# Kernel tuning notes

Measured on AMD Instinct MI355X. Metric: run time of the kernel, lower is better.

The kernel has to match this reference:

```python
import jax, jax.numpy as jnp
import numpy as np

N_TOKENS = 100000
CUT = [0, 20000, 50000, 100000]  # cutoff_ends
D = 1024


def setup_inputs() -> dict:
    key = jax.random.key(0)
    ks = jax.random.split(key, 12)
    B, S = 2, 1024
    hidden = jax.random.normal(ks[0], (B, S, D), dtype=jnp.float32)
    target = jax.random.randint(ks[1], (B, S), 0, N_TOKENS, dtype=jnp.int64)
    s = 0.02
    # cluster 0 (shortlist) + cluster projection head
    w0 = jax.random.normal(ks[2], (20000, 1024), dtype=jnp.float32) * s
    b0 = jnp.zeros((20000,), jnp.float32)
    cluster_w = jax.random.normal(ks[3], (2, 1024), dtype=jnp.float32) * s  # n_clusters=2
    cluster_b = jnp.zeros((2,), jnp.float32)
    proj0 = jax.random.normal(ks[4], (1024, 1024), dtype=jnp.float32) * s  # d_proj x d_emb_0
    # tail cluster 1: d_emb_1 = 1024 // 4 = 256, vocab slice 20000..50000
    w1 = jax.random.normal(ks[5], (30000, 256), dtype=jnp.float32) * s
    b1 = jnp.zeros((30000,), jnp.float32)
    proj1 = jax.random.normal(ks[6], (1024, 256), dtype=jnp.float32) * s
    # tail cluster 2: d_emb_2 = 1024 // 16 = 64, vocab slice 50000..100000
    w2 = jax.random.normal(ks[7], (50000, 64), dtype=jnp.float32) * s
    b2 = jnp.zeros((50000,), jnp.float32)
    proj2 = jax.random.normal(ks[8], (1024, 64), dtype=jnp.float32) * s
    return {"hidden": hidden, "target": target,
            "w0": w0, "b0": b0, "cluster_w": cluster_w, "cluster_b": cluster_b, "proj0": proj0,
            "w1": w1, "b1": b1, "proj1": proj1,
            "w2": w2, "b2": b2, "proj2": proj2}


def reference(hidden, target, w0, b0, cluster_w, cluster_b, proj0,
              w1, b1, proj1, w2, b2, proj2):
    tgt_shape = target.shape
    h = hidden.reshape(-1, D)            # [N, d_proj]
    t = target.reshape(-1)               # [N]

    # head: shortlist logits + cluster logits, via low-rank projection
    head_w = jnp.concatenate([w0, cluster_w], axis=0)   # [20002, 1024]
    head_b = jnp.concatenate([b0, cluster_b], axis=0)
    head_logit = (h @ proj0) @ head_w.T + head_b        # [N, 20002]
    head_lp = jax.nn.log_softmax(head_logit, axis=1)

    nll = jnp.zeros(t.shape, h.dtype)

    # cluster 0 (shortlist): logprob is head_lp at the target id
    m0 = t < CUT[1]
    idx0 = jnp.clip(t, 0, CUT[1] - 1)
    lp0 = jnp.take_along_axis(head_lp, idx0[:, None], axis=1)[:, 0]
    nll = jnp.where(m0, -lp0, nll)

    # tail clusters. NOTE: faithful to original quirk head_logprob[:, -i]
    tails = [(CUT[1], CUT[2], w1, b1, proj1), (CUT[2], CUT[3], w2, b2, proj2)]
    for i, (left, right, w, b, p) in enumerate(tails, start=1):
        m = (t >= left) & (t < right)
        tail_logit = (h @ p) @ w.T + b                  # [N, right-left]
        tail_lp = jax.nn.log_softmax(tail_logit, axis=1)
        ti = jnp.clip(t - left, 0, right - left - 1)
        lp = head_lp[:, -i] + jnp.take_along_axis(tail_lp, ti[:, None], axis=1)[:, 0]
        nll = jnp.where(m, -lp, nll)

    return nll.reshape(tgt_shape)
```

## Files before the change

### kernel.cpp

```cpp
#include <hip/hip_runtime.h>
#include <cstdint>
#include <cstddef>

#define DEV static __device__ __forceinline__

typedef __attribute__((ext_vector_type(8))) short bf16x8_t;
typedef __attribute__((ext_vector_type(4))) float f32x4_t;

DEV unsigned short f2bf(float f) {
  union { float f; unsigned u; } v; v.f = f;
  unsigned r = v.u + 0x7fffu + ((v.u >> 16) & 1u);
  return (unsigned short)(r >> 16);
}

DEV void gl_lds16(const void* g, void* l) {
  __builtin_amdgcn_global_load_lds(
      (const __attribute__((address_space(1))) void*)g,
      (__attribute__((address_space(3))) void*)l,
      16, 0, 0);
}

__global__ __launch_bounds__(256)
void prep_k(const int* __restrict__ target,
            int* __restrict__ idx1, int* __restrict__ pos1,
            int* __restrict__ idx2, int* __restrict__ pos2,
            int* __restrict__ cnts,
            const float* __restrict__ p0, const float* __restrict__ p1,
            const float* __restrict__ p2, unsigned short* __restrict__ pAll,
            const float* __restrict__ s0, unsigned short* __restrict__ d0, int n0,
            const float* __restrict__ s1, unsigned short* __restrict__ d1, int n1,
            const float* __restrict__ s2, unsigned short* __restrict__ d2, int n2,
            const float* __restrict__ s3, unsigned short* __restrict__ d3, int n3,
            const float* __restrict__ s4, unsigned short* __restrict__ d4, int n4) {
  const int bid = blockIdx.x;
  const int tid = threadIdx.x;
  if (bid == 0) {
    __shared__ int c1, c2;
    if (tid == 0) { c1 = 0; c2 = 0; }
    __syncthreads();
    for (int i = tid; i < 2048; i += 256) {
      int t = target[i];
      if (t >= 20000 && t < 50000) {
        int p = atomicAdd(&c1, 1); idx1[p] = i; pos1[i] = p;
      } else if (t >= 50000) {
        int p = atomicAdd(&c2, 1); idx2[p] = i; pos2[i] = p;
      }
    }
    __syncthreads();
    if (tid == 0) { cnts[0] = c1; cnts[1] = c2; }
    return;
  }
  if (bid <= 1344) {
    __shared__ float tile[32][33];
    int b = bid - 1;
    const float* src; unsigned short* dst; int C, bx, by;
    if (b < 1024)      { src = p0; dst = pAll;               C = 1024; bx = b % 32; by = b / 32; }
    else if (b < 1280) { int q = b - 1024; src = p1; dst = pAll + 1024 * 1024; C = 256; bx = q % 8; by = q / 8; }
    else               { int q = b - 1280; src = p2; dst = pAll + 1280 * 1024; C = 64;  bx = q % 2; by = q / 2; }
    const int R = 1024;
    int tx = tid & 31, ty = tid >> 5;
    int c0 = bx * 32, r0 = by * 32;
    for (int yy = ty; yy < 32; yy += 8)
      tile[yy][tx] = src[(size_t)(r0 + yy) * C + (c0 + tx)];
    __syncthreads();
    for (int yy = ty; yy < 32; yy += 8)
      dst[(size_t)(c0 + yy) * R + (r0 + tx)] = f2bf(tile[tx][yy]);
    return;
  }
  int j = (bid - 1345) * 256 + tid;
  const float* s; unsigned short* d;
  if (j < n0) { s = s0; d = d0; }
  else { j -= n0;
    if (j < n1) { s = s1; d = d1; }
    else { j -= n1;
      if (j < n2) { s = s2; d = d2; }
      else { j -= n2;
        if (j < n3) { s = s3; d = d3; }
        else { j -= n3; if (j >= n4) return; s = s4; d = d4; }
      }
    }
  }
  float4 f = ((const float4*)s)[j];
  ushort4 o;
  o.x = f2bf(f.x); o.y = f2bf(f.y); o.z = f2bf(f.z); o.w = f2bf(f.w);
  ((ushort4*)d)[j] = o;
}

__global__ __launch_bounds__(256)
void proj_gemm_k(const unsigned short* __restrict__ A,
                 const unsigned short* __restrict__ W,
                 unsigned short* __restrict__ Cout) {
  __shared__ __align__(16) unsigned short As[128 * 32];
  __shared__ __align__(16) unsigned short Bs[128 * 32];
  const int K = 1024, V = 1344;
  const int tm = blockIdx.x, tn = blockIdx.y;
  const int m0 = tm * 128, n0 = tn * 128;
  const int tid = threadIdx.x, wid = tid >> 6, lane = tid & 63;
  const int quad = lane >> 4, l16 = lane & 15;
  const int wr = wid >> 1, wc = wid & 1;

  f32x4_t acc[4][4];
  const f32x4_t zero4 = {0.f, 0.f, 0.f, 0.f};
#pragma unroll
  for (int i = 0; i < 4; ++i)
#pragma unroll
    for (int j = 0; j < 4; ++j) acc[i][j] = zero4;

  const int srow = wid * 32 + (lane >> 2);
  const int skk  = (lane & 3) * 8;
  const unsigned short* Ap0 = A + (size_t)(m0 + srow) * K + skk;
  const unsigned short* Ap1 = A + (size_t)(m0 + srow + 16) * K + skk;
  int wrow0 = n0 + srow;      if (wrow0 > V - 1) wrow0 = V - 1;
  int wrow1 = n0 + srow + 16; if (wrow1 > V - 1) wrow1 = V - 1;
  const unsigned short* Wp0 = W + (size_t)wrow0 * K + skk;
  const unsigned short* Wp1 = W + (size_t)wrow1 * K + skk;
  unsigned short* Asw = As + wid * 1024;
  unsigned short* Bsw = Bs + wid * 1024;

  for (int k0 = 0; k0 < K; k0 += 32) {
    gl_lds16(Ap0, Asw);
    gl_lds16(Ap1, Asw + 512);
    gl_lds16(Wp0, Bsw);
    gl_lds16(Wp1, Bsw + 512);
    Ap0 += 32; Ap1 += 32; Wp0 += 32; Wp1 += 32;
    __syncthreads();
    bf16x8_t af[4], bfr[4];
#pragma unroll
    for (int i = 0; i < 4; ++i)
      af[i] = *(const bf16x8_t*)(As + (size_t)(wr * 64 + i * 16 + l16) * 32 + quad * 8);
#pragma unroll
    for (int j = 0; j < 4; ++j)
      bfr[j] = *(const bf16x8_t*)(Bs + (size_t)(wc * 64 + j * 16 + l16) * 32 + quad * 8);
#pragma unroll
    for (int i = 0; i < 4; ++i)
#pragma unroll
      for (int j = 0; j < 4; ++j)
        acc[i][j] = __builtin_amdgcn_mfma_f32_16x16x32_bf16(af[i], bfr[j], acc[i][j], 0, 0, 0);
    __syncthreads();
  }
#pragma unroll
  for (int i = 0; i < 4; ++i)
#pragma unroll
    for (int j = 0; j < 4; ++j) {
      const int n = n0 + wc * 64 + j * 16 + l16;
      if (n < V) {
#pragma unroll
        for (int r = 0; r < 4; ++r) {
          const int m = m0 + wr * 64 + i * 16 + quad * 4 + r;
          Cout[(size_t)m * V + n] = f2bf(acc[i][j][r]);
        }
      }
    }
}


#define SBAR() __builtin_amdgcn_s_barrier()

#define STA(BUF, HALF, KT)                                                    \
  {                                                                           \
    const unsigned short* g_ = aB0 + (size_t)(HALF) * (128 * 1344) + (KT) * 64; \
    char* d_ = (char*)SA[BUF][HALF] + ldsw;                                   \
    gl_lds16(g_, d_);                                                         \
    gl_lds16(g_ + 64 * 1344, d_ + 8192);                                      \
  }

#define STB(BUF, HALF, KT)                                                    \
  {                                                                           \
    char* d_ = (char*)SB[BUF][HALF] + ldsw;                                   \
    gl_lds16(bP##HALF##0 + (KT) * 64, d_);                                    \
    gl_lds16(bP##HALF##1 + (KT) * 64, d_ + 8192);                             \
  }

#define MMQ(mb, nb, BB)                                                       \
  {                                                                           \
    _Pragma("unroll") for (int mi = 0; mi < 4; ++mi) {                        \
      _Pragma("unroll") for (int nj = 0; nj < 2; ++nj) {                      \
        acc[(mb) + mi][(nb) + nj] = __builtin_amdgcn_mfma_f32_16x16x32_bf16(  \
            Af[0][mi], BB[0][nj], acc[(mb) + mi][(nb) + nj], 0, 0, 0);        \
        acc[(mb) + mi][(nb) + nj] = __builtin_amdgcn_mfma_f32_16x16x32_bf16(  \
            Af[1][mi], BB[1][nj], acc[(mb) + mi][(nb) + nj], 0, 0, 0);        \
      }                                                                       \
    }                                                                         \
  }

#define PH(D_, E_, KTV)                                                       \
  {                                                                           \
    const int kt_ = (KTV);                                                    \
    const int t1_ = (kt_ + 1 > 15) ? 15 : (kt_ + 1);                          \
    const int t2_ = (kt_ + 2 > 15) ? 15 : (kt_ + 2);                          \
              \
    _Pragma("unroll") for (int mi = 0; mi < 4; ++mi) {                        \
      Af[0][mi] = *(const bf16x8_t*)(pa##D_##a + mi * 2048);                  \
      Af[1][mi] = *(const bf16x8_t*)(pa##D_##b + mi * 2048);                  \
    }                                                                         \
    _Pragma("unroll") for (int nj = 0; nj < 2; ++nj) {                        \
      Bh[0][nj] = *(const bf16x8_t*)(pb##D_##a + (2 + nj) * 2048);            \
      Bh[1][nj] = *(const bf16x8_t*)(pb##D_##b + (2 + nj) * 2048);            \
    }                                                                         \
    STB(E_, 1, t1_);                                                          \
    __builtin_amdgcn_s_setprio(1); MMQ(0, 0, Bl); __builtin_amdgcn_s_setprio(0); \
    SBAR();                                                                   \
              \
    __builtin_amdgcn_s_setprio(1); MMQ(0, 2, Bh); __builtin_amdgcn_s_setprio(0); \
    _Pragma("unroll") for (int mi = 0; mi < 4; ++mi) {                        \
      Af[0][mi] = *(const bf16x8_t*)(pa##D_##a + (4 + mi) * 2048);            \
      Af[1][mi] = *(const bf16x8_t*)(pa##D_##b + (4 + mi) * 2048);            \
    }                                                                         \
    STA(E_, 1, t1_);                                                          \
    SBAR();                                                                   \
               \
    STB(D_, 0, t2_);                                                          \
    __builtin_amdgcn_s_setprio(1); MMQ(4, 0, Bl); __builtin_amdgcn_s_setprio(0); \
    asm volatile("s_waitcnt vmcnt(2)" ::: "memory");                          \
    SBAR();                                                                   \
           \
    STA(D_, 0, t2_);                                                          \
    _Pragma("unroll") for (int nj = 0; nj < 2; ++nj) {                        \
      Bl[0][nj] = *(const bf16x8_t*)(pb##E_##a + nj * 2048);                  \
      Bl[1][nj] = *(const bf16x8_t*)(pb##E_##b + nj * 2048);                  \
    }                                                                         \
    __builtin_amdgcn_s_setprio(1); MMQ(4, 2, Bh); __builtin_amdgcn_s_setprio(0); \
    SBAR();                                                                   \
  }

#define PROLOGUE6()                                                           \
  { STB(0, 0, 0); STA(0, 0, 0); STB(0, 1, 0); STA(0, 1, 0);                   \
    STB(1, 0, 1); STA(1, 0, 1); }

typedef unsigned short lds_half_t[2][8192];

DEV void head_body(char* UB, int bid,
                   const unsigned short* __restrict__ Pall,
                   const unsigned short* __restrict__ w0b,
                   const float* __restrict__ b0, const float* __restrict__ cb,
                   float* __restrict__ part0, float* __restrict__ g0,
                   float* __restrict__ cg, const int* __restrict__ target) {
  lds_half_t* SA = (lds_half_t*)UB;
  lds_half_t* SB = (lds_half_t*)(UB + 65536);

  const int V = 20002;
  const int orig = (bid & 7) * 79 + (bid >> 3);
  const int mt = orig & 7, stripe = orig >> 3;
  const int m0 = mt * 256, n0 = stripe * 256;

  const int tid = threadIdx.x;
  const int wid = tid >> 6, lane = tid & 63;
  const int quad = lane >> 4, l16 = lane & 15;
  const int wr = wid >> 2, wc = wid & 3;

  const int r0  = tid >> 3;
  const int ibh = ((tid & 7) ^ (r0 & 7)) << 3;

  const unsigned short* aB0 = Pall + (size_t)(m0 + r0) * 1344 + ibh;
  int br00 = n0 + r0;            if (br00 > V - 1) br00 = V - 1;
  int br01 = n0 + r0 + 64;       if (br01 > V - 1) br01 = V - 1;
  int br10 = n0 + 128 + r0;      if (br10 > V - 1) br10 = V - 1;
  int br11 = n0 + 128 + r0 + 64; if (br11 > V - 1) br11 = V - 1;
  const unsigned short* bP00 = w0b + (size_t)br00 * 1024 + ibh;
  const unsigned short* bP01 = w0b + (size_t)br01 * 1024 + ibh;
  const unsigned short* bP10 = w0b + (size_t)br10 * 1024 + ibh;
  const unsigned short* bP11 = w0b + (size_t)br11 * 1024 + ibh;

  const int ldsw = wid * 1024;

  const int aoff0 = l16 * 128 + ((quad ^ (l16 & 3)) << 4) + (((l16 >> 2) & 1) << 6);
  const int aoff1 = aoff0 ^ 64;
  const char* pa0a = (const char*)SA[0][wr] + aoff0;
  const char* pa0b = (const char*)SA[0][wr] + aoff1;
  const char* pa1a = (const char*)SA[1][wr] + aoff0;
  const char* pa1b = (const char*)SA[1][wr] + aoff1;
  const char* pb0a = (const char*)SB[0][wc >> 1] + (wc & 1) * 8192 + aoff0;
  const char* pb0b = (const char*)SB[0][wc >> 1] + (wc & 1) * 8192 + aoff1;
  const char* pb1a = (const char*)SB[1][wc >> 1] + (wc & 1) * 8192 + aoff0;
  const char* pb1b = (const char*)SB[1][wc >> 1] + (wc & 1) * 8192 + aoff1;

  f32x4_t acc[8][4];
  const f32x4_t zero4 = {0.f, 0.f, 0.f, 0.f};
#pragma unroll
  for (int i = 0; i < 8; ++i)
#pragma unroll
    for (int j = 0; j < 4; ++j) acc[i][j] = zero4;

  bf16x8_t Af[2][4];
  bf16x8_t Bl[2][2];
  bf16x8_t Bh[2][2];

  PROLOGUE6();
  asm volatile("s_waitcnt vmcnt(4)" ::: "memory");
  SBAR();
#pragma unroll
  for (int nj = 0; nj < 2; ++nj) {
    Bl[0][nj] = *(const bf16x8_t*)(pb0a + nj * 2048);
    Bl[1][nj] = *(const bf16x8_t*)(pb0b + nj * 2048);
  }

#pragma unroll 1
  for (int ktp = 0; ktp < 8; ++ktp) {
    const int kt0 = 2 * ktp;
    PH(0, 1, kt0);
    PH(1, 0, kt0 + 1);
  }

  asm volatile("s_waitcnt vmcnt(0) lgkmcnt(0)" ::: "memory");
  SBAR();

  int nj[4]; float bj[4];
#pragma unroll
  for (int j = 0; j < 4; ++j) {
    nj[j] = n0 + wc * 64 + j * 16 + l16;
    bj[j] = (nj[j] < 20000) ? b0[nj[j]] : ((nj[j] < V) ? cb[nj[j] - 20000] : 0.f);
  }
  float* redf = (float*)UB;
#pragma unroll
  for (int i = 0; i < 8; ++i) {
#pragma unroll
    for (int r = 0; r < 4; ++r) {
      const int rloc = i * 16 + quad * 4 + r;
      const int token = m0 + wr * 128 + rloc;
      float v[4], sum = 0.f;
#pragma unroll
      for (int j = 0; j < 4; ++j) {
        v[j] = acc[i][j][r] + bj[j];
        if (nj[j] < V) sum += __expf(v[j]);
      }
#pragma unroll
      for (int off = 1; off < 16; off <<= 1)
        sum += __shfl_xor(sum, off, 64);
      if (l16 == 0) redf[(wr * 4 + wc) * 128 + rloc] = sum;
      const int t = target[token];
      const int gi = (t < 19999) ? t : 19999;
#pragma unroll
      for (int j = 0; j < 4; ++j) {
        if (nj[j] == gi) g0[token] = v[j];
        if (nj[j] == 20000) cg[2 * token]     = v[j];
        if (nj[j] == 20001) cg[2 * token + 1] = v[j];
      }
    }
  }
  __syncthreads();
  if (tid < 256) {
    const int wrr = tid >> 7, rr = tid & 127;
    const float s = redf[(wrr * 4 + 0) * 128 + rr] + redf[(wrr * 4 + 1) * 128 + rr]
                  + redf[(wrr * 4 + 2) * 128 + rr] + redf[(wrr * 4 + 3) * 128 + rr];
    part0[(size_t)(m0 + tid) * 79 + stripe] = s;
  }
}

#undef PH
#undef MMQ
#undef STA
#undef STB
#undef PROLOGUE6
#undef SBAR

template <int KT>
DEV void tail_body8(char* UB, int tn,
                    const unsigned short* __restrict__ A, int ldA,
                    const unsigned short* __restrict__ W,
                    const float* __restrict__ bias, int V, int nt2x,
                    const int* __restrict__ rowidx,
                    const int* __restrict__ cnt_ptr,
                    float* __restrict__ partials,
                    float* __restrict__ gathered,
                    const int* __restrict__ target, int glo) {
  constexpr int KC  = KT / 64;
  constexpr int NCB = KT / 32;
  unsigned short* Bs = (unsigned short*)UB;
  char* AsB = UB + NCB * 8192;

  const int n0 = tn * 128;
  const int Meff = *cnt_ptr;
  const int tid = threadIdx.x;
  const int lane = tid & 63, wid = tid >> 6;
  const int quad = lane >> 4, l16 = lane & 15;
  const int wr = wid >> 1, wc = wid & 1;
  const int srow = tid >> 2;
  const int scol = (tid & 3) * 8;
  const int ldsw = wid * 1024;

  int wrow = n0 + srow; if (wrow > V - 1) wrow = V - 1;
#pragma unroll
  for (int c = 0; c < NCB; ++c)
    gl_lds16(W + (size_t)wrow * KT + c * 32 + scol, (char*)Bs + c * 8192 + ldsw);

  int nj[4]; float bj[4];
#pragma unroll
  for (int j = 0; j < 4; ++j) {
    nj[j] = n0 + wc * 64 + j * 16 + l16;
    bj[j] = (nj[j] < V) ? bias[nj[j]] : 0.f;
  }

  const int nm = (Meff + 255) >> 8;
  const int S = nm * KC;

  auto stageA = [&](int s, int buf) {
    const int m = s / KC, k = s - m * KC;
#pragma unroll
    for (int cc = 0; cc < 2; ++cc)
#pragma unroll
      for (int h = 0; h < 2; ++h) {
        int ar = m * 256 + srow + h * 128;
        if (ar > Meff - 1) ar = Meff - 1;
        if (ar < 0) ar = 0;
        const int Arow = rowidx[ar];
        gl_lds16(A + (size_t)Arow * ldA + k * 64 + cc * 32 + scol,
                 AsB + buf * 32768 + cc * 16384 + h * 8192 + ldsw);
      }
  };

  stageA(0, 0);
  __syncthreads();

  f32x4_t acc[4][4];
  const f32x4_t zero4 = {0.f, 0.f, 0.f, 0.f};

  for (int s = 0; s < S; ++s) {
    const int buf = s & 1;
    const int m = s / KC, k = s - m * KC;
    if (s + 1 < S) stageA(s + 1, buf ^ 1);
    if (k == 0) {
#pragma unroll
      for (int i = 0; i < 4; ++i)
#pragma unroll
        for (int j = 0; j < 4; ++j) acc[i][j] = zero4;
    }
#pragma unroll
    for (int cc = 0; cc < 2; ++cc) {
      bf16x8_t af[4], bfr[4];
#pragma unroll
      for (int i = 0; i < 4; ++i)
        af[i] = *(const bf16x8_t*)(AsB + buf * 32768 + cc * 16384 +
                                   (wr * 64 + i * 16 + l16) * 64 + quad * 16);
#pragma unroll
      for (int j = 0; j < 4; ++j)
        bfr[j] = *(const bf16x8_t*)((char*)Bs + (k * 2 + cc) * 8192 +
                                    (wc * 64 + j * 16 + l16) * 64 + quad * 16);
#pragma unroll
      for (int i = 0; i < 4; ++i)
#pragma unroll
        for (int j = 0; j < 4; ++j)
          acc[i][j] = __builtin_amdgcn_mfma_f32_16x16x32_bf16(af[i], bfr[j], acc[i][j], 0, 0, 0);
    }
    if (k == KC - 1) {
#pragma unroll
      for (int i = 0; i < 4; ++i) {
#pragma unroll
        for (int r = 0; r < 4; ++r) {
          const int row = wr * 64 + i * 16 + quad * 4 + r;
          const int gr = m * 256 + row;
          const int grc = (gr < Meff) ? gr : (Meff - 1);
          const int token = rowidx[grc];
          float v[4], sum = 0.f;
#pragma unroll
          for (int j = 0; j < 4; ++j) {
            v[j] = acc[i][j][r] + bj[j];
            if (nj[j] < V) sum += __expf(v[j]);
          }
#pragma unroll
          for (int off = 1; off < 16; off <<= 1)
            sum += __shfl_xor(sum, off, 64);
          if (l16 == 0)
            partials[(size_t)grc * nt2x + 2 * tn + wc] = sum;
          const int gi = target[token] - glo;
#pragma unroll
          for (int j = 0; j < 4; ++j)
            if (nj[j] == gi) gathered[token] = v[j];
        }
      }
    }
    __syncthreads();
  }
}

__global__ __launch_bounds__(512, 2)
void fused_k(const unsigned short* __restrict__ Pall,
             const unsigned short* __restrict__ w0b,
             const float* __restrict__ b0, const float* __restrict__ cb,
             float* __restrict__ part0, float* __restrict__ g0,
             float* __restrict__ cg, const int* __restrict__ target,
             const unsigned short* __restrict__ w1b, const float* __restrict__ b1,
             const int* __restrict__ idx1, const int* __restrict__ cnt1,
             float* __restrict__ part1, float* __restrict__ g1,
             const unsigned short* __restrict__ w2b, const float* __restrict__ b2,
             const int* __restrict__ idx2, const int* __restrict__ cnt2,
             float* __restrict__ part2, float* __restrict__ g2,
             int nt1x2, int nt2x2) {
  __shared__ __align__(16) char UB[132096];
  const int bid = blockIdx.x;
  if (bid < 632) {
    head_body(UB, bid, Pall, w0b, b0, cb, part0, g0, cg, target);
  } else if (bid < 632 + 235) {
    tail_body8<256>(UB, bid - 632, Pall + 1024, 1344, w1b, b1, 30000, nt1x2,
                    idx1, cnt1, part1, g1, target, 20000);
  } else {
    tail_body8<64>(UB, bid - 867, Pall + 1280, 1344, w2b, b2, 50000, nt2x2,
                   idx2, cnt2, part2, g2, target, 50000);
  }
}

__global__ __launch_bounds__(256)
void combine_k(const float* __restrict__ part0,
               const float* __restrict__ part1, int nt1,
               const float* __restrict__ part2, int nt2,
               const float* __restrict__ g0, const float* __restrict__ g1,
               const float* __restrict__ g2, const float* __restrict__ cg,
               const int* __restrict__ pos1, const int* __restrict__ pos2,
               const int* __restrict__ target, float* __restrict__ out) {
  const int w = threadIdx.x >> 6, lane = threadIdx.x & 63;
  const int token = blockIdx.x * 4 + w;
  const int t = target[token];

  float S = 0.f;
  for (int i = lane; i < 79; i += 64)
    S += part0[(size_t)token * 79 + i];
#pragma unroll
  for (int off = 1; off < 64; off <<= 1)
    S += __shfl_xor(S, off, 64);
  const float lse_head = __logf(S);

  float res;
  if (t < 20000) {
    res = lse_head - g0[token];
  } else {
    const float* pt; int nt; float gv, ch; int row;
    if (t < 50000) { pt = part1; nt = nt1; gv = g1[token]; ch = cg[2 * token + 1]; row = pos1[token]; }
    else           { pt = part2; nt = nt2; gv = g2[token]; ch = cg[2 * token];     row = pos2[token]; }
    float S2 = 0.f;
    for (int i = lane; i < nt; i += 64)
      S2 += pt[(size_t)row * nt + i];
#pragma unroll
    for (int off = 1; off < 64; off <<= 1)
      S2 += __shfl_xor(S2, off, 64);
    float lse_t = __logf(S2);
    res = -((ch - lse_head) + (gv - lse_t));
  }
  if (lane == 0) out[token] = res;
}

extern "C" void kernel_launch(void* const* d_in, const int* in_sizes, int n_in,
                              void* d_out, int out_size, void* d_ws, size_t ws_size,
                              hipStream_t stream) {
  (void)in_sizes; (void)n_in; (void)out_size; (void)ws_size;
  const float* hidden = (const float*)d_in[0];
  const int*   target = (const int*)d_in[1];
  const float* w0     = (const float*)d_in[2];
  const float* b0     = (const float*)d_in[3];
  const float* cw     = (const float*)d_in[4];
  const float* cb     = (const float*)d_in[5];
  const float* proj0  = (const float*)d_in[6];
  const float* w1     = (const float*)d_in[7];
  const float* b1     = (const float*)d_in[8];
  const float* proj1  = (const float*)d_in[9];
  const float* w2     = (const float*)d_in[10];
  const float* b2     = (const float*)d_in[11];
  const float* proj2  = (const float*)d_in[12];
  float* out = (float*)d_out;

  const int NT1 = 235, NT2 = 391;
  const int NT1X = 2 * NT1, NT2X = 2 * NT2;

  char* p = (char*)d_ws;
  auto alloc = [&](size_t bytes) {
    char* r = p; p += (bytes + 255) & ~(size_t)255; return r;
  };
  unsigned short* Hb   = (unsigned short*)alloc(2048ull * 1024 * 2);
  unsigned short* pAll = (unsigned short*)alloc(1344ull * 1024 * 2);
  unsigned short* w0b  = (unsigned short*)alloc(20002ull * 1024 * 2);
  unsigned short* w1b  = (unsigned short*)alloc(30000ull * 256 * 2);
  unsigned short* w2b  = (unsigned short*)alloc(50000ull * 64 * 2);
  unsigned short* Pall = (unsigned short*)alloc(2048ull * 1344 * 2);
  float* part0 = (float*)alloc(2048ull * 79 * 4);
  float* part1 = (float*)alloc(2048ull * NT1X * 4);
  float* part2 = (float*)alloc(2048ull * NT2X * 4);
  float* g0 = (float*)alloc(2048 * 4);
  float* g1 = (float*)alloc(2048 * 4);
  float* g2 = (float*)alloc(2048 * 4);
  float* cg = (float*)alloc(2048 * 2 * 4);
  int* idx1 = (int*)alloc(2048 * 4);
  int* pos1 = (int*)alloc(2048 * 4);
  int* idx2 = (int*)alloc(2048 * 4);
  int* pos2 = (int*)alloc(2048 * 4);
  int* cnts = (int*)alloc(2 * 4);

  const int c_h = 2048 * 1024 / 4, c_w0 = 20000 * 1024 / 4, c_cw = 2048 / 4,
            c_w1 = 30000 * 256 / 4, c_w2 = 50000 * 64 / 4;
  const int ctot = c_h + c_w0 + c_cw + c_w1 + c_w2;
  const int nb_cast = (ctot + 255) / 256;
  prep_k<<<1 + 1344 + nb_cast, 256, 0, stream>>>(
      target, idx1, pos1, idx2, pos2, cnts,
      proj0, proj1, proj2, pAll,
      hidden, Hb, c_h,
      w0, w0b, c_w0,
      cw, w0b + 20000ull * 1024, c_cw,
      w1, w1b, c_w1,
      w2, w2b, c_w2);

  proj_gemm_k<<<dim3(16, 11), 256, 0, stream>>>(Hb, pAll, Pall);

  fused_k<<<632 + NT1 + NT2, 512, 0, stream>>>(
      Pall, w0b, b0, cb, part0, g0, cg, target,
      w1b, b1, idx1, cnts + 0, part1, g1,
      w2b, b2, idx2, cnts + 1, part2, g2,
      NT1X, NT2X);

  combine_k<<<512, 256, 0, stream>>>(part0, part1, NT1X, part2, NT2X,
      g0, g1, g2, cg, pos1, pos2, target, out);
}
```

Before: 384.2 us.

## Overlap weight casts with projection GEMM and fold combine into fused kernel

Moves the bf16 casting of the vocabulary weights out of the prep kernel and into the projection GEMM launch as extra blocks, so the casts run alongside the GEMM instead of before it. Replaces the separate combine kernel with a tail in fused_k: each block takes a ticket from an atomic counter, and the last 32 blocks spin until all blocks finish, then do the per-token log-sum-exp combine. This removes one launch and one inter-kernel gap. It relies on the last-ticket blocks being resident while they wait, and on NB=1258 matching the actual grid size, which depends on NT1/NT2.

```diff
diff --git a/kernel.cpp b/kernel.cpp
--- a/kernel.cpp
+++ b/kernel.cpp
@@ -27,11 +27,7 @@
             int* __restrict__ cnts,
             const float* __restrict__ p0, const float* __restrict__ p1,
             const float* __restrict__ p2, unsigned short* __restrict__ pAll,
-            const float* __restrict__ s0, unsigned short* __restrict__ d0, int n0,
-            const float* __restrict__ s1, unsigned short* __restrict__ d1, int n1,
-            const float* __restrict__ s2, unsigned short* __restrict__ d2, int n2,
-            const float* __restrict__ s3, unsigned short* __restrict__ d3, int n3,
-            const float* __restrict__ s4, unsigned short* __restrict__ d4, int n4) {
+            const float* __restrict__ s0, unsigned short* __restrict__ d0, int n0) {
   const int bid = blockIdx.x;
   const int tid = threadIdx.x;
   if (bid == 0) {
@@ -47,7 +43,7 @@
       }
     }
     __syncthreads();
-    if (tid == 0) { cnts[0] = c1; cnts[1] = c2; }
+    if (tid == 0) { cnts[0] = c1; cnts[1] = c2; cnts[2] = 0; }
     return;
   }
   if (bid <= 1344) {
@@ -68,34 +64,47 @@
     return;
   }
   int j = (bid - 1345) * 256 + tid;
-  const float* s; unsigned short* d;
-  if (j < n0) { s = s0; d = d0; }
-  else { j -= n0;
-    if (j < n1) { s = s1; d = d1; }
-    else { j -= n1;
-      if (j < n2) { s = s2; d = d2; }
-      else { j -= n2;
-        if (j < n3) { s = s3; d = d3; }
-        else { j -= n3; if (j >= n4) return; s = s4; d = d4; }
-      }
-    }
-  }
-  float4 f = ((const float4*)s)[j];
+  if (j >= n0) return;
+  float4 f = ((const float4*)s0)[j];
   ushort4 o;
   o.x = f2bf(f.x); o.y = f2bf(f.y); o.z = f2bf(f.z); o.w = f2bf(f.w);
-  ((ushort4*)d)[j] = o;
+  ((ushort4*)d0)[j] = o;
 }
 
 __global__ __launch_bounds__(256)
-void proj_gemm_k(const unsigned short* __restrict__ A,
-                 const unsigned short* __restrict__ W,
-                 unsigned short* __restrict__ Cout) {
+void projcast_k(const unsigned short* __restrict__ A,
+                const unsigned short* __restrict__ W,
+                unsigned short* __restrict__ Cout,
+                const float* __restrict__ s0, unsigned short* __restrict__ d0, int n0,
+                const float* __restrict__ s1, unsigned short* __restrict__ d1, int n1,
+                const float* __restrict__ s2, unsigned short* __restrict__ d2, int n2,
+                const float* __restrict__ s3, unsigned short* __restrict__ d3, int n3) {
+  const int bid = blockIdx.x;
+  const int tid = threadIdx.x;
+  if (bid >= 176) {
+    int j = (bid - 176) * 256 + tid;
+    const float* s; unsigned short* d;
+    if (j < n0) { s = s0; d = d0; }
+    else { j -= n0;
+      if (j < n1) { s = s1; d = d1; }
+      else { j -= n1;
+        if (j < n2) { s = s2; d = d2; }
+        else { j -= n2; if (j >= n3) return; s = s3; d = d3; }
+      }
+    }
+    float4 f = ((const float4*)s)[j];
+    ushort4 o;
+    o.x = f2bf(f.x); o.y = f2bf(f.y); o.z = f2bf(f.z); o.w = f2bf(f.w);
+    ((ushort4*)d)[j] = o;
+    return;
+  }
+
   __shared__ __align__(16) unsigned short As[128 * 32];
   __shared__ __align__(16) unsigned short Bs[128 * 32];
   const int K = 1024, V = 1344;
-  const int tm = blockIdx.x, tn = blockIdx.y;
-  const int m0 = tm * 128, n0 = tn * 128;
-  const int tid = threadIdx.x, wid = tid >> 6, lane = tid & 63;
+  const int tm = bid & 15, tn = bid >> 4;
+  const int m0 = tm * 128, n0g = tn * 128;
+  const int wid = tid >> 6, lane = tid & 63;
   const int quad = lane >> 4, l16 = lane & 15;
   const int wr = wid >> 1, wc = wid & 1;
 
@@ -110,8 +119,8 @@
   const int skk  = (lane & 3) * 8;
   const unsigned short* Ap0 = A + (size_t)(m0 + srow) * K + skk;
   const unsigned short* Ap1 = A + (size_t)(m0 + srow + 16) * K + skk;
-  int wrow0 = n0 + srow;      if (wrow0 > V - 1) wrow0 = V - 1;
-  int wrow1 = n0 + srow + 16; if (wrow1 > V - 1) wrow1 = V - 1;
+  int wrow0 = n0g + srow;      if (wrow0 > V - 1) wrow0 = V - 1;
+  int wrow1 = n0g + srow + 16; if (wrow1 > V - 1) wrow1 = V - 1;
   const unsigned short* Wp0 = W + (size_t)wrow0 * K + skk;
   const unsigned short* Wp1 = W + (size_t)wrow1 * K + skk;
   unsigned short* Asw = As + wid * 1024;
@@ -142,7 +151,7 @@
   for (int i = 0; i < 4; ++i)
 #pragma unroll
     for (int j = 0; j < 4; ++j) {
-      const int n = n0 + wc * 64 + j * 16 + l16;
+      const int n = n0g + wc * 64 + j * 16 + l16;
       if (n < V) {
 #pragma unroll
         for (int r = 0; r < 4; ++r) {
@@ -188,7 +197,6 @@
     const int kt_ = (KTV);                                                    \
     const int t1_ = (kt_ + 1 > 15) ? 15 : (kt_ + 1);                          \
     const int t2_ = (kt_ + 2 > 15) ? 15 : (kt_ + 2);                          \
-              \
     _Pragma("unroll") for (int mi = 0; mi < 4; ++mi) {                        \
       Af[0][mi] = *(const bf16x8_t*)(pa##D_##a + mi * 2048);                  \
       Af[1][mi] = *(const bf16x8_t*)(pa##D_##b + mi * 2048);                  \
@@ -200,7 +208,6 @@
     STB(E_, 1, t1_);                                                          \
     __builtin_amdgcn_s_setprio(1); MMQ(0, 0, Bl); __builtin_amdgcn_s_setprio(0); \
     SBAR();                                                                   \
-              \
     __builtin_amdgcn_s_setprio(1); MMQ(0, 2, Bh); __builtin_amdgcn_s_setprio(0); \
     _Pragma("unroll") for (int mi = 0; mi < 4; ++mi) {                        \
       Af[0][mi] = *(const bf16x8_t*)(pa##D_##a + (4 + mi) * 2048);            \
@@ -208,12 +215,10 @@
     }                                                                         \
     STA(E_, 1, t1_);                                                          \
     SBAR();                                                                   \
-               \
     STB(D_, 0, t2_);                                                          \
     __builtin_amdgcn_s_setprio(1); MMQ(4, 0, Bl); __builtin_amdgcn_s_setprio(0); \
     asm volatile("s_waitcnt vmcnt(2)" ::: "memory");                          \
     SBAR();                                                                   \
-           \
     STA(D_, 0, t2_);                                                          \
     _Pragma("unroll") for (int nj = 0; nj < 2; ++nj) {                        \
       Bl[0][nj] = *(const bf16x8_t*)(pb##E_##a + nj * 2048);                  \
@@ -472,6 +477,47 @@
   }
 }
 
+DEV void combine_body(int ci,
+                      const float* __restrict__ part0,
+                      const float* __restrict__ part1, int nt1,
+                      const float* __restrict__ part2, int nt2,
+                      const float* __restrict__ g0, const float* __restrict__ g1,
+                      const float* __restrict__ g2, const float* __restrict__ cg,
+                      const int* __restrict__ pos1, const int* __restrict__ pos2,
+                      const int* __restrict__ target, float* __restrict__ out) {
+  const int wid = threadIdx.x >> 6, lane = threadIdx.x & 63;
+  for (int s = 0; s < 8; ++s) {
+    const int token = ci * 64 + wid * 8 + s;
+    const int t = target[token];
+
+    float S = 0.f;
+    for (int i = lane; i < 79; i += 64)
+      S += part0[(size_t)token * 79 + i];
+#pragma unroll
+    for (int off = 1; off < 64; off <<= 1)
+      S += __shfl_xor(S, off, 64);
+    const float lse_head = __logf(S);
+
+    float res;
+    if (t < 20000) {
+      res = lse_head - g0[token];
+    } else {
+      const float* pt; int nt; float gv, ch; int row;
+      if (t < 50000) { pt = part1; nt = nt1; gv = g1[token]; ch = cg[2 * token + 1]; row = pos1[token]; }
+      else           { pt = part2; nt = nt2; gv = g2[token]; ch = cg[2 * token];     row = pos2[token]; }
+      float S2 = 0.f;
+      for (int i = lane; i < nt; i += 64)
+        S2 += pt[(size_t)row * nt + i];
+#pragma unroll
+      for (int off = 1; off < 64; off <<= 1)
+        S2 += __shfl_xor(S2, off, 64);
+      float lse_t = __logf(S2);
+      res = -((ch - lse_head) + (gv - lse_t));
+    }
+    if (lane == 0) out[token] = res;
+  }
+}
+
 __global__ __launch_bounds__(512, 2)
 void fused_k(const unsigned short* __restrict__ Pall,
              const unsigned short* __restrict__ w0b,
@@ -484,7 +530,10 @@
              const unsigned short* __restrict__ w2b, const float* __restrict__ b2,
              const int* __restrict__ idx2, const int* __restrict__ cnt2,
              float* __restrict__ part2, float* __restrict__ g2,
-             int nt1x2, int nt2x2) {
+             int nt1x2, int nt2x2,
+             int* __restrict__ done,
+             const int* __restrict__ pos1, const int* __restrict__ pos2,
+             float* __restrict__ out) {
   __shared__ __align__(16) char UB[132096];
   const int bid = blockIdx.x;
   if (bid < 632) {
@@ -496,45 +545,24 @@
     tail_body8<64>(UB, bid - 867, Pall + 1280, 1344, w2b, b2, 50000, nt2x2,
                    idx2, cnt2, part2, g2, target, 50000);
   }
-}
-
-__global__ __launch_bounds__(256)
-void combine_k(const float* __restrict__ part0,
-               const float* __restrict__ part1, int nt1,
-               const float* __restrict__ part2, int nt2,
-               const float* __restrict__ g0, const float* __restrict__ g1,
-               const float* __restrict__ g2, const float* __restrict__ cg,
-               const int* __restrict__ pos1, const int* __restrict__ pos2,
-               const int* __restrict__ target, float* __restrict__ out) {
-  const int w = threadIdx.x >> 6, lane = threadIdx.x & 63;
-  const int token = blockIdx.x * 4 + w;
-  const int t = target[token];
-
-  float S = 0.f;
-  for (int i = lane; i < 79; i += 64)
-    S += part0[(size_t)token * 79 + i];
-#pragma unroll
-  for (int off = 1; off < 64; off <<= 1)
-    S += __shfl_xor(S, off, 64);
-  const float lse_head = __logf(S);
-
-  float res;
-  if (t < 20000) {
-    res = lse_head - g0[token];
-  } else {
-    const float* pt; int nt; float gv, ch; int row;
-    if (t < 50000) { pt = part1; nt = nt1; gv = g1[token]; ch = cg[2 * token + 1]; row = pos1[token]; }
-    else           { pt = part2; nt = nt2; gv = g2[token]; ch = cg[2 * token];     row = pos2[token]; }
-    float S2 = 0.f;
-    for (int i = lane; i < nt; i += 64)
-      S2 += pt[(size_t)row * nt + i];
-#pragma unroll
-    for (int off = 1; off < 64; off <<= 1)
-      S2 += __shfl_xor(S2, off, 64);
-    float lse_t = __logf(S2);
-    res = -((ch - lse_head) + (gv - lse_t));
-  }
-  if (lane == 0) out[token] = res;
+
+  const int NB = 1258, NC = 32;
+  __shared__ int tkt;
+  __syncthreads();
+  if (threadIdx.x == 0) {
+    __threadfence();
+    tkt = atomicAdd(done, 1);
+  }
+  __syncthreads();
+  const int t = tkt;
+  if (t < NB - NC) return;
+  if (threadIdx.x == 0) {
+    while (atomicAdd(done, 0) < NB) __builtin_amdgcn_s_sleep(8);
+  }
+  __syncthreads();
+  __threadfence();
+  combine_body(t - (NB - NC), part0, part1, nt1x2, part2, nt2x2,
+               g0, g1, g2, cg, pos1, pos2, target, out);
 }
 
 extern "C" void kernel_launch(void* const* d_in, const int* in_sizes, int n_in,
@@ -580,29 +608,29 @@
   int* pos1 = (int*)alloc(2048 * 4);
   int* idx2 = (int*)alloc(2048 * 4);
   int* pos2 = (int*)alloc(2048 * 4);
-  int* cnts = (int*)alloc(2 * 4);
-
-  const int c_h = 2048 * 1024 / 4, c_w0 = 20000 * 1024 / 4, c_cw = 2048 / 4,
-            c_w1 = 30000 * 256 / 4, c_w2 = 50000 * 64 / 4;
-  const int ctot = c_h + c_w0 + c_cw + c_w1 + c_w2;
-  const int nb_cast = (ctot + 255) / 256;
-  prep_k<<<1 + 1344 + nb_cast, 256, 0, stream>>>(
+  int* cnts = (int*)alloc(4 * 4);
+
+  const int c_h = 2048 * 1024 / 4;
+  prep_k<<<1 + 1344 + c_h / 256, 256, 0, stream>>>(
       target, idx1, pos1, idx2, pos2, cnts,
       proj0, proj1, proj2, pAll,
-      hidden, Hb, c_h,
+      hidden, Hb, c_h);
+
+  const int c_w0 = 20000 * 1024 / 4, c_cw = 2048 / 4,
+            c_w1 = 30000 * 256 / 4, c_w2 = 50000 * 64 / 4;
+  const int ctot = c_w0 + c_cw + c_w1 + c_w2;
+  const int nb_cast = (ctot + 255) / 256;
+  projcast_k<<<176 + nb_cast, 256, 0, stream>>>(
+      Hb, pAll, Pall,
       w0, w0b, c_w0,
       cw, w0b + 20000ull * 1024, c_cw,
       w1, w1b, c_w1,
       w2, w2b, c_w2);
 
-  proj_gemm_k<<<dim3(16, 11), 256, 0, stream>>>(Hb, pAll, Pall);
-
   fused_k<<<632 + NT1 + NT2, 512, 0, stream>>>(
       Pall, w0b, b0, cb, part0, g0, cg, target,
       w1b, b1, idx1, cnts + 0, part1, g1,
       w2b, b2, idx2, cnts + 1, part2, g2,
-      NT1X, NT2X);
-
-  combine_k<<<512, 256, 0, stream>>>(part0, part1, NT1X, part2, NT2X,
-      g0, g1, g2, cg, pos1, pos2, target, out);
-}
+      NT1X, NT2X,
+      cnts + 2, pos1, pos2, out);
+}
```

New measurement: 475.8 us. 1.24x slower.
